# Kernel tuning notes

Hardware: AMD Instinct MI355X
Metric: run time of the kernel (lower is better)

The kernel has to match this reference:

```python
import jax, jax.numpy as jnp
import numpy as np

B, C, L, V, H, HEADS, ITERS = 8, 2048, 3, 512, 256, 8, 8
HD = H // HEADS
MAX_LIT = 1024  # literal embedding table holds 2*MAX_LIT rows


def _lin(x, W, b):
    return x @ W.T + b


def _gelu(x):
    return jax.nn.gelu(x, approximate=False)  # torch nn.GELU default = exact erf


def _ln(x, g, b):
    m = x.mean(-1, keepdims=True)
    v = ((x - m) ** 2).mean(-1, keepdims=True)
    return (x - m) / jnp.sqrt(v + 1e-5) * g + b


def setup_inputs() -> dict:
    key = jax.random.key(0)
    ks = jax.random.split(key, 16)
    s = 0.02
    p = {}
    p["formula"] = jax.random.randint(ks[0], (B, C, L), 0, 2 * V)
    p["lit_emb"] = jax.random.normal(ks[1], (2 * MAX_LIT, H)) * s
    # clause_encoder: Linear(H,2H) -> LayerNorm(2H) -> GELU -> Linear(2H,H)
    p["ce_w1"] = jax.random.normal(ks[2], (2 * H, H)) * s
    p["ce_b1"] = jnp.zeros((2 * H,))
    p["ce_g"] = jnp.ones((2 * H,))
    p["ce_beta"] = jnp.zeros((2 * H,))
    p["ce_w2"] = jax.random.normal(ks[3], (H, 2 * H)) * s
    p["ce_b2"] = jnp.zeros((H,))
    # clause_var_attention (nn.MultiheadAttention, eval mode -> no dropout)
    p["attn_in_w"] = jax.random.normal(ks[4], (3 * H, H)) * s
    p["attn_in_b"] = jnp.zeros((3 * H,))
    p["attn_out_w"] = jax.random.normal(ks[5], (H, H)) * s
    p["attn_out_b"] = jnp.zeros((H,))
    # variable_selector: Linear -> GELU -> Linear(H,1)
    p["vs_w1"] = jax.random.normal(ks[6], (H, H)) * s
    p["vs_b1"] = jnp.zeros((H,))
    p["vs_w2"] = jax.random.normal(ks[7], (1, H)) * s
    p["vs_b2"] = jnp.zeros((1,))
    # assignment_predictor: Linear -> GELU -> Linear(H,2) -> Softmax
    p["ap_w1"] = jax.random.normal(ks[8], (H, H)) * s
    p["ap_b1"] = jnp.zeros((H,))
    p["ap_w2"] = jax.random.normal(ks[9], (2, H)) * s
    p["ap_b2"] = jnp.zeros((2,))
    # sat_predictor: Linear -> GELU -> Linear(H,1) -> Sigmoid
    p["sp_w1"] = jax.random.normal(ks[10], (H, H)) * s
    p["sp_b1"] = jnp.zeros((H,))
    p["sp_w2"] = jax.random.normal(ks[11], (1, H)) * s
    p["sp_b2"] = jnp.zeros((1,))
    return p


def _mha(q, kv, in_w, in_b, out_w, out_b):
    Wq, Wk, Wv = jnp.split(in_w, 3, axis=0)
    bq, bk, bv = jnp.split(in_b, 3, axis=0)
    Bq, Nq, _ = q.shape
    Nk = kv.shape[1]
    qh = _lin(q, Wq, bq).reshape(Bq, Nq, HEADS, HD).transpose(0, 2, 1, 3)
    kh = _lin(kv, Wk, bk).reshape(Bq, Nk, HEADS, HD).transpose(0, 2, 1, 3)
    vh = _lin(kv, Wv, bv).reshape(Bq, Nk, HEADS, HD).transpose(0, 2, 1, 3)
    attn = jax.nn.softmax(jnp.einsum("bhqd,bhkd->bhqk", qh, kh) / np.float32(np.sqrt(HD)), axis=-1)
    o = jnp.einsum("bhqk,bhkd->bhqd", attn, vh).transpose(0, 2, 1, 3).reshape(Bq, Nq, H)
    return _lin(o, out_w, out_b)


def reference(formula, lit_emb, ce_w1, ce_b1, ce_g, ce_beta, ce_w2, ce_b2,
              attn_in_w, attn_in_b, attn_out_w, attn_out_b,
              vs_w1, vs_b1, vs_w2, vs_b2, ap_w1, ap_b1, ap_w2, ap_b2,
              sp_w1, sp_b1, sp_w2, sp_b2):
    bidx = jnp.arange(B)
    lit_e = lit_emb[formula]  # [B,C,L,H]
    # clause_encoder output is assignment-independent -> hoist out of the loop
    base = _lin(_gelu(_ln(_lin(lit_e.mean(2), ce_w1, ce_b1), ce_g, ce_beta)), ce_w2, ce_b2)  # [B,C,H]
    var_idx = formula // 2  # [B,C,L]
    pol = formula % 2

    def step(carry, _):
        assignments, var_states, done = carry
        va = assignments[bidx[:, None, None], var_idx]          # [B,C,L] gather
        sat = jnp.any((va == pol) & (va != 2), -1)              # [B,C]
        clause_states = base * (1.0 - 0.9 * sat[..., None].astype(base.dtype))
        vs = _mha(var_states, clause_states, attn_in_w, attn_in_b, attn_out_w, attn_out_b)  # [B,V,H]
        scores = _lin(_gelu(_lin(vs, vs_w1, vs_b1)), vs_w2, vs_b2)[..., 0]  # [B,V]
        scores = scores + (assignments != 2).astype(scores.dtype) * (-1e9)
        sel = jnp.argmax(scores, 1)                             # [B]
        sel_states = vs[bidx, sel]
        probs = jax.nn.softmax(_lin(_gelu(_lin(sel_states, ap_w1, ap_b1)), ap_w2, ap_b2), -1)
        new_a = jnp.argmax(probs, 1).astype(assignments.dtype)
        a2 = assignments.at[bidx, sel].set(new_a)
        # conflict check with updated assignments
        va2 = a2[bidx[:, None, None], var_idx]
        sat2 = jnp.any((va2 == pol) & (va2 != 2), -1)
        conflicting = jnp.all(va2 != 2, -1) & ~sat2             # [B,C]
        any_conf = jnp.any(conflicting)                         # global, as in torch list check
        a3 = jnp.where(any_conf, a2.at[bidx, sel].set(2), a2)   # unassign selected var on conflict
        finished = jnp.all(a3 != 2) & ~any_conf                 # torch early-break condition
        assignments_n = jnp.where(done, assignments, a3)        # freeze after break
        vs_n = jnp.where(done, var_states, vs)
        return (assignments_n, vs_n, done | finished), None

    init = (jnp.full((B, V), 2, jnp.int32), jnp.zeros((B, V, H), base.dtype), jnp.array(False))
    (assignments, var_states, _), _ = jax.lax.scan(step, init, None, length=ITERS)
    is_sat = jax.nn.sigmoid(_lin(_gelu(_lin(var_states.mean(1), sp_w1, sp_b1)), sp_w2, sp_b2))  # [B,1]
    return is_sat, assignments
```

## Files before the change

### kernel.cpp

```cpp
#include <hip/hip_runtime.h>
#include <hip/hip_bf16.h>

#pragma clang fp contract(off)

#define DEVI __device__ __forceinline__

constexpr int Bc = 8, Cc = 2048, Vc = 512, Hc = 256;

constexpr int W_N = 23;
constexpr int W_OFF[W_N] = {
  0,        524288,  655360,  655872,  656384,  656896,  787968,  788224,
  984832,   985600,  1051136, 1051392, 1116928, 1117184, 1117440, 1117444,
  1182980,  1183236, 1183748, 1183752, 1249288, 1249544, 1249800 };
constexpr int W_SZ[W_N] = {
  524288, 131072, 512, 512, 512, 131072, 256, 196608, 768,
  65536, 256, 65536, 256, 256, 1, 65536, 256, 512, 2, 65536, 256, 256, 1 };
constexpr int W_TOT = 1249804;

constexpr size_t WT1_O   = 1249808;
constexpr size_t WT2_O   = WT1_O   + 131072;
constexpr size_t WTIN_O  = WT2_O   + 131072;
constexpr size_t WTOUT_O = WTIN_O  + 196608;
constexpr size_t WTV1_O  = WTOUT_O + 65536;
constexpr size_t WTAP_O  = WTV1_O  + 65536;
constexpr size_t WTSP_O  = WTAP_O  + 65536;
constexpr size_t WCK_O   = WTSP_O  + 65536;
constexpr size_t WCV_O   = WCK_O   + 131072;
constexpr size_t BCK_O   = WCV_O   + 131072;
constexpr size_t BCV_O   = BCK_O   + 256;
constexpr size_t KB_O    = BCV_O   + 256;
constexpr size_t VB_O    = KB_O    + 4194304;
constexpr size_t VS8_O   = VB_O    + 4194304;
constexpr size_t OP_O    = VS8_O   + 2048;
constexpr size_t PM_O    = OP_O    + 8192;
constexpr size_t PL_O    = PM_O    + 256;
constexpr size_t FTOT    = PL_O    + 256;

constexpr int T_N = 7;
constexpr int T_SRC[T_N]  = { 524288, 656896, 788224, 985600, 1051392, 1117444, 1183752 };
constexpr size_t T_DST[T_N] = { WT1_O, WT2_O, WTIN_O, WTOUT_O, WTV1_O, WTAP_O, WTSP_O };
constexpr int T_ROWS[T_N] = { 512, 256, 768, 256, 256, 256, 256 };
constexpr int T_L2C[T_N]  = { 8, 9, 8, 8, 8, 8, 8 };
constexpr int T_CUM[T_N + 1] = { 0, 131072, 262144, 458752, 524288, 589824, 655360, 720896 };

struct SrcPtrs { const void* p[W_N]; };

DEVI float gelu_ref(float x) {
  return (x * (erff(x / 1.41421356237309504880f) + 1.0f)) * 0.5f;
}

__global__ __launch_bounds__(256) void k_detect(const unsigned short* __restrict__ lit,
                                                int* __restrict__ dflag) {
  __shared__ int red[256];
  int t = threadIdx.x, c = 0;
  for (int i = t; i < 4096; i += 256) {
    unsigned e = (lit[i] >> 7) & 0xFF;
    if (e >= 0x8F) c++;
  }
  red[t] = c;
  __syncthreads();
  for (int s = 128; s > 0; s >>= 1) {
    if (t < s) red[t] += red[t + s];
    __syncthreads();
  }
  if (t == 0) dflag[0] = (red[0] > 64) ? 1 : 0;
}

__global__ __launch_bounds__(256) void k_convert(SrcPtrs sp, float* __restrict__ wf,
                                                 const int* __restrict__ dflag) {
  int idx = blockIdx.x * 256 + threadIdx.x;
  if (idx >= W_TOT) return;
  const int isf32 = dflag[0];
  int i = 0;
  while (i + 1 < W_N && idx >= W_OFF[i + 1]) i++;
  int j = idx - W_OFF[i];
  float v = 0.f;
  if (j < W_SZ[i]) {
    if (isf32) v = ((const float*)sp.p[i])[j];
    else {
      unsigned int u = (unsigned int)((const unsigned short*)sp.p[i])[j] << 16;
      v = __uint_as_float(u);
    }
  }
  wf[idx] = v;
}

__global__ __launch_bounds__(256) void k_transpose(float* __restrict__ wf) {
  int idx = blockIdx.x * 256 + threadIdx.x;
  if (idx >= T_CUM[T_N]) return;
  int mi = 0;
  while (mi + 1 < T_N && idx >= T_CUM[mi + 1]) mi++;
  int local = idx - T_CUM[mi];
  int cols = 1 << T_L2C[mi];
  int r = local >> T_L2C[mi];
  int c = local & (cols - 1);
  wf[T_DST[mi] + (size_t)c * T_ROWS[mi] + r] = wf[T_SRC[mi] + (size_t)local];
}

__global__ __launch_bounds__(256) void k_combine(float* __restrict__ wf) {
  const int blk = blockIdx.x, t = threadIdx.x;
  const float* wtin = wf + WTIN_O;
  if (blk < 512) {
    __shared__ float w2row[256];
    w2row[t] = wf[WT2_O + (size_t)blk * 256 + t];
    __syncthreads();
    float aK = 0.f, aV = 0.f;
    for (int m = 0; m < 256; ++m) {
      float w2 = w2row[m];
      aK = fmaf(w2, wtin[(size_t)m * 768 + 256 + t], aK);
      aV = fmaf(w2, wtin[(size_t)m * 768 + 512 + t], aV);
    }
    wf[WCK_O + (size_t)blk * 256 + t] = aK;
    wf[WCV_O + (size_t)blk * 256 + t] = aV;
  } else {
    float aK = 0.f, aV = 0.f;
    for (int m = 0; m < 256; ++m) {
      float b2 = wf[W_OFF[6] + m];
      aK = fmaf(b2, wtin[(size_t)m * 768 + 256 + t], aK);
      aV = fmaf(b2, wtin[(size_t)m * 768 + 512 + t], aV);
    }
    wf[BCK_O + t] = aK;
    wf[BCV_O + t] = aV;
  }
}

__global__ __launch_bounds__(256) void k_init(float* __restrict__ vs8,
    int* __restrict__ assign, int* __restrict__ flags) {
  int idx = blockIdx.x * 256 + threadIdx.x;
  assign[idx] = 2;
  if (idx < 2048) vs8[idx] = 0.f;
  if (idx < 4) flags[idx] = 0;
}

__global__ __launch_bounds__(256) void k_base(const int* __restrict__ formula,
    const float* __restrict__ wf, float* __restrict__ Kb, float* __restrict__ Vb) {
  __shared__ __align__(16) float xs[16][256];
  __shared__ __align__(16) float h1[16][516];
  __shared__ float mv[16], vr[16];
  const int t = threadIdx.x;
  const int n0 = blockIdx.x * 16;
  const float* lit = wf + W_OFF[0];
  for (int r = 0; r < 16; ++r) {
    int n = n0 + r;
    int f0 = formula[n*3+0], f1 = formula[n*3+1], f2 = formula[n*3+2];
    xs[r][t] = (lit[f0*256 + t] + lit[f1*256 + t] + lit[f2*256 + t]) / 3.0f;
  }
  __syncthreads();
  {
    const float* w1t = wf + WT1_O;
    float a0[16], a1[16];
    #pragma unroll
    for (int r = 0; r < 16; ++r) { a0[r] = 0.f; a1[r] = 0.f; }
    for (int k = 0; k < 256; k += 4) {
      float wa0 = w1t[(size_t)(k+0)*512 + t], wa1 = w1t[(size_t)(k+1)*512 + t];
      float wa2 = w1t[(size_t)(k+2)*512 + t], wa3 = w1t[(size_t)(k+3)*512 + t];
      float wb0 = w1t[(size_t)(k+0)*512 + 256 + t], wb1 = w1t[(size_t)(k+1)*512 + 256 + t];
      float wb2 = w1t[(size_t)(k+2)*512 + 256 + t], wb3 = w1t[(size_t)(k+3)*512 + 256 + t];
      #pragma unroll
      for (int r = 0; r < 16; ++r) {
        float4 x4 = *(const float4*)&xs[r][k];
        a0[r] = fmaf(x4.x, wa0, a0[r]);
        a0[r] = fmaf(x4.y, wa1, a0[r]);
        a0[r] = fmaf(x4.z, wa2, a0[r]);
        a0[r] = fmaf(x4.w, wa3, a0[r]);
        a1[r] = fmaf(x4.x, wb0, a1[r]);
        a1[r] = fmaf(x4.y, wb1, a1[r]);
        a1[r] = fmaf(x4.z, wb2, a1[r]);
        a1[r] = fmaf(x4.w, wb3, a1[r]);
      }
    }
    float b0 = wf[W_OFF[2] + t], b1b = wf[W_OFF[2] + t + 256];
    #pragma unroll
    for (int r = 0; r < 16; ++r) {
      h1[r][t] = a0[r] + b0;
      h1[r][t + 256] = a1[r] + b1b;
    }
  }
  __syncthreads();
  if (t < 16) {
    float s = 0.f;
    for (int k = 0; k < 512; ++k) s += h1[t][k];
    float m = s / 512.0f;
    float v = 0.f;
    for (int k = 0; k < 512; ++k) { float d = h1[t][k] - m; float d2 = d * d; v += d2; }
    mv[t] = m; vr[t] = v / 512.0f;
  }
  __syncthreads();
  {
    const float* g  = wf + W_OFF[3];
    const float* be = wf + W_OFF[4];
    for (int r = 0; r < 16; ++r) {
      float sd = sqrtf(vr[r] + 1e-5f);
      for (int c = t; c < 512; c += 256) {
        float val = (h1[r][c] - mv[r]) / sd * g[c] + be[c];
        h1[r][c] = gelu_ref(val);
      }
    }
  }
  __syncthreads();
  {
    const float* wck = wf + WCK_O;
    const float* wcv = wf + WCV_O;
    float aK[16], aV[16];
    #pragma unroll
    for (int r = 0; r < 16; ++r) { aK[r] = 0.f; aV[r] = 0.f; }
    for (int k = 0; k < 512; k += 4) {
      float ck0 = wck[(size_t)(k+0)*256 + t], ck1 = wck[(size_t)(k+1)*256 + t];
      float ck2 = wck[(size_t)(k+2)*256 + t], ck3 = wck[(size_t)(k+3)*256 + t];
      float cv0 = wcv[(size_t)(k+0)*256 + t], cv1 = wcv[(size_t)(k+1)*256 + t];
      float cv2 = wcv[(size_t)(k+2)*256 + t], cv3 = wcv[(size_t)(k+3)*256 + t];
      #pragma unroll
      for (int r = 0; r < 16; ++r) {
        float4 x4 = *(const float4*)&h1[r][k];
        aK[r] = fmaf(x4.x, ck0, aK[r]);
        aK[r] = fmaf(x4.y, ck1, aK[r]);
        aK[r] = fmaf(x4.z, ck2, aK[r]);
        aK[r] = fmaf(x4.w, ck3, aK[r]);
        aV[r] = fmaf(x4.x, cv0, aV[r]);
        aV[r] = fmaf(x4.y, cv1, aV[r]);
        aV[r] = fmaf(x4.z, cv2, aV[r]);
        aV[r] = fmaf(x4.w, cv3, aV[r]);
      }
    }
    float bck = wf[BCK_O + t], bcv = wf[BCV_O + t];
    const int h = t >> 5, d = t & 31;
    for (int r = 0; r < 16; ++r) {
      int n = n0 + r;
      int b = n >> 11, j = n & 2047;
      size_t off = ((size_t)(b * 8 + h) * 2048 + j) * 32 + d;
      Kb[off] = aK[r] + bck;
      Vb[off] = aV[r] + bcv;
    }
  }
}

__global__ __launch_bounds__(256) void k_attn_part(const int* __restrict__ formula,
    const int* __restrict__ assign, const float* __restrict__ Kb,
    const float* __restrict__ Vb, const float* __restrict__ wf,
    const float* __restrict__ vs8, float* __restrict__ op, float* __restrict__ pm,
    float* __restrict__ pl, const int* __restrict__ flags) {
  if (flags[0]) return;
  __shared__ float xv[256], qs[32];
  __shared__ float sS[512], sF[512];
  __shared__ float sRed[256];
  __shared__ float sO[8][32];
  __shared__ float sM, sQB;
  const int blk = blockIdx.x;
  const int bh = blk >> 2, c = blk & 3;
  const int b = bh >> 3, h = bh & 7;
  const int t = threadIdx.x;
  const float FAC1 = 1.0f - 0.9f;

  xv[t] = vs8[b * 256 + t];
  __syncthreads();
  if (t < 32) {
    const float* wt = wf + WTIN_O;
    const int cc = h * 32 + t;
    float acc = 0.f;
    for (int k = 0; k < 256; ++k) acc = fmaf(xv[k], wt[(size_t)k * 768 + cc], acc);
    qs[t] = acc + wf[W_OFF[8] + cc];
  }
  __syncthreads();
  if (t == 0) {
    const float* bk = wf + W_OFF[8] + 256;
    float s = 0.f;
    for (int d = 0; d < 32; ++d) s = fmaf(qs[d], bk[h * 32 + d], s);
    sQB = s;
  }
  __syncthreads();
  float qreg[32];
  #pragma unroll
  for (int d = 0; d < 32; ++d) qreg[d] = qs[d];
  const float qb = sQB;
  const float* kbh = Kb + (size_t)bh * 2048 * 32;
  const float* vbh = Vb + (size_t)bh * 2048 * 32;

  float mloc = -3.402823466e38f;
  #pragma unroll
  for (int i = 0; i < 2; ++i) {
    int jl = i * 256 + t;
    int j = c * 512 + jl;
    int n = b * 2048 + j;
    bool sat = false;
    #pragma unroll
    for (int l = 0; l < 3; ++l) {
      int f = formula[n * 3 + l];
      int a = assign[b * 512 + (f >> 1)];
      sat = sat || (a == (f & 1));
    }
    float fac = sat ? FAC1 : 1.0f;
    const float4* kr4 = (const float4*)(kbh + (size_t)j * 32);
    float p = 0.f;
    #pragma unroll
    for (int g = 0; g < 8; ++g) {
      float4 kk = kr4[g];
      p = fmaf(qreg[4*g+0], kk.x, p);
      p = fmaf(qreg[4*g+1], kk.y, p);
      p = fmaf(qreg[4*g+2], kk.z, p);
      p = fmaf(qreg[4*g+3], kk.w, p);
    }
    float s = fmaf(fac, p, qb);
    sS[jl] = s; sF[jl] = fac;
    mloc = fmaxf(mloc, s);
  }
  sRed[t] = mloc;
  __syncthreads();
  for (int st = 128; st > 0; st >>= 1) {
    if (t < st) sRed[t] = fmaxf(sRed[t], sRed[t + st]);
    __syncthreads();
  }
  if (t == 0) sM = sRed[0];
  __syncthreads();
  const float Mc = sM;

  {
    float u0 = expf(sS[t * 2] - Mc);
    float u1 = expf(sS[t * 2 + 1] - Mc);
    float ll = u0 + u1;
    sS[t * 2] = u0 * sF[t * 2];
    sS[t * 2 + 1] = u1 * sF[t * 2 + 1];
    __syncthreads();
    sRed[t] = ll;
    __syncthreads();
    for (int st = 128; st > 0; st >>= 1) {
      if (t < st) sRed[t] = sRed[t] + sRed[t + st];
      __syncthreads();
    }
  }
  {
    const int jg = t >> 5, d = t & 31;
    float acc = 0.f;
    const float* vbase = vbh + (size_t)(c * 512 + jg * 64) * 32 + d;
    for (int jj = 0; jj < 64; ++jj)
      acc = fmaf(sS[jg * 64 + jj], vbase[(size_t)jj * 32], acc);
    sO[jg][d] = acc;
  }
  __syncthreads();
  if (t < 32) {
    float o = sO[0][t];
    #pragma unroll
    for (int g = 1; g < 8; ++g) o += sO[g][t];
    op[(size_t)(bh * 4 + c) * 32 + t] = o;
    if (t == 0) { pm[bh * 4 + c] = Mc; pl[bh * 4 + c] = sRed[0]; }
  }
}

__global__ __launch_bounds__(256) void k_update(const int* __restrict__ formula,
    const float* __restrict__ op, const float* __restrict__ pm,
    const float* __restrict__ pl, const float* __restrict__ wf,
    float* __restrict__ vs8, int* __restrict__ assign, int* __restrict__ selb,
    int* __restrict__ flags) {
  if (flags[0]) return;
  const int b = blockIdx.x, t = threadIdx.x;
  __shared__ float xo[256], xv[256], hh[256];
  __shared__ int ssel, sna, sconf, suna, slast;
  if (t == 0) { ssel = 512; sconf = 0; suna = 0; }
  {
    const int h = t >> 5, d = t & 31, bh = b * 8 + h;
    float m0 = pm[bh*4+0], m1 = pm[bh*4+1], m2 = pm[bh*4+2], m3 = pm[bh*4+3];
    float M = fmaxf(fmaxf(m0, m1), fmaxf(m2, m3));
    float e0 = expf(m0 - M), e1 = expf(m1 - M), e2 = expf(m2 - M), e3 = expf(m3 - M);
    float den = e0 * pl[bh*4+0];
    den = fmaf(e1, pl[bh*4+1], den);
    den = fmaf(e2, pl[bh*4+2], den);
    den = fmaf(e3, pl[bh*4+3], den);
    float O = e0 * op[(size_t)(bh*4+0)*32 + d];
    O = fmaf(e1, op[(size_t)(bh*4+1)*32 + d], O);
    O = fmaf(e2, op[(size_t)(bh*4+2)*32 + d], O);
    O = fmaf(e3, op[(size_t)(bh*4+3)*32 + d], O);
    float bv = wf[W_OFF[8] + 512 + h * 32 + d];
    xo[h * 32 + d] = O / den + bv;
  }
  __syncthreads();
  {
    const float* wt = wf + WTOUT_O;
    float acc = 0.f;
    for (int k = 0; k < 256; ++k) acc = fmaf(xo[k], wt[(size_t)k * 256 + t], acc);
    float v = acc + wf[W_OFF[10] + t];
    vs8[b * 256 + t] = v;
    xv[t] = v;
  }
  __syncthreads();
  for (int i = t; i < 512; i += 256)
    if (assign[b * 512 + i] == 2) atomicMin(&ssel, i);
  __syncthreads();
  const int sel = (ssel == 512) ? 0 : ssel;
  {
    const float* wt = wf + WTAP_O;
    float a = 0.f;
    for (int k = 0; k < 256; ++k) a = fmaf(xv[k], wt[(size_t)k * 256 + t], a);
    hh[t] = gelu_ref(a + wf[W_OFF[16] + t]);
  }
  __syncthreads();
  if (t == 0) {
    const float* w2 = wf + W_OFF[17];
    float l0 = 0.f, l1 = 0.f;
    for (int k = 0; k < 256; ++k) l0 = fmaf(hh[k], w2[k], l0);
    for (int k = 0; k < 256; ++k) l1 = fmaf(hh[k], w2[256 + k], l1);
    l0 += wf[W_OFF[18]];
    l1 += wf[W_OFF[18] + 1];
    int na = (l1 > l0) ? 1 : 0;
    assign[b * 512 + sel] = na;
    selb[b] = sel;
    sna = na;
  }
  __syncthreads();
  const int na = sna;
  int conf = 0, una = 0;
  for (int i = t; i < 2048; i += 256) {
    int n = b * 2048 + i;
    bool sat = false, alla = true;
    #pragma unroll
    for (int l = 0; l < 3; ++l) {
      int f = formula[n * 3 + l];
      int v = f >> 1;
      int a = (v == sel) ? na : assign[b * 512 + v];
      sat = sat || (a == (f & 1));
      alla = alla && (a != 2);
    }
    if (alla && !sat) conf = 1;
  }
  for (int i = t; i < 512; i += 256) {
    int a = (i == sel) ? na : assign[b * 512 + i];
    if (a == 2) una = 1;
  }
  if (conf) atomicOr(&sconf, 1);
  if (una) atomicOr(&suna, 1);
  __syncthreads();
  if (t == 0) {
    if (sconf) atomicOr(&flags[1], 1);
    if (suna) atomicOr(&flags[2], 1);
    __threadfence();
    int old = atomicAdd(&flags[3], 1);
    slast = (old == 7) ? 1 : 0;
  }
  __syncthreads();
  if (slast) {
    __threadfence();
    const int ac = flags[1], ua = flags[2];
    if (ac && t < 8) assign[t * 512 + selb[t]] = 2;
    if (t == 0) {
      if (!ac && !ua) flags[0] = 1;
      flags[1] = 0;
      flags[2] = 0;
      flags[3] = 0;
    }
  }
}

__global__ __launch_bounds__(256) void k_issat(const float* __restrict__ vs8,
    const int* __restrict__ assign, const float* __restrict__ wf,
    void* __restrict__ outv, const int* __restrict__ dflag) {
  const int b = blockIdx.x, t = threadIdx.x;
  const int isf32 = dflag[0];
  __shared__ float x[256], h[256];
  x[t] = vs8[b * 256 + t];
  __syncthreads();
  const float* wt = wf + WTSP_O;
  float a = 0.f;
  for (int k = 0; k < 256; ++k) a = fmaf(x[k], wt[(size_t)k * 256 + t], a);
  h[t] = gelu_ref(a + wf[W_OFF[20] + t]);
  __syncthreads();
  if (t == 0) {
    const float* w2 = wf + W_OFF[21];
    float l = 0.f;
    for (int k = 0; k < 256; ++k) l = fmaf(h[k], w2[k], l);
    l += wf[W_OFF[22]];
    float sig = 1.f / (1.f + expf(-l));
    if (isf32) ((float*)outv)[b] = sig;
    else ((__hip_bfloat16*)outv)[b] = __float2bfloat16(sig);
  }
  for (int i = t; i < 512; i += 256) {
    float av = (float)assign[b * 512 + i];
    if (isf32) ((float*)outv)[8 + b * 512 + i] = av;
    else ((__hip_bfloat16*)outv)[8 + b * 512 + i] = __float2bfloat16(av);
  }
}

extern "C" void kernel_launch(void* const* d_in, const int* in_sizes, int n_in,
                              void* d_out, int out_size, void* d_ws, size_t ws_size,
                              hipStream_t stream) {
  (void)in_sizes; (void)n_in; (void)out_size; (void)ws_size;
  const int* formula = (const int*)d_in[0];
  float* wf = (float*)d_ws;
  SrcPtrs sp;
  for (int i = 0; i < W_N; ++i) sp.p[i] = d_in[i + 1];
  float* Kb   = wf + KB_O;
  float* Vb   = wf + VB_O;
  float* vs8  = wf + VS8_O;
  float* op   = wf + OP_O;
  float* pm   = wf + PM_O;
  float* pl   = wf + PL_O;
  int* iw     = (int*)(wf + FTOT);
  int* assign = iw;
  int* selb   = iw + 4096;
  int* flags  = iw + 4104;
  int* dflag  = iw + 4108;

  k_detect<<<1, 256, 0, stream>>>((const unsigned short*)d_in[1], dflag);
  k_convert<<<(W_TOT + 255) / 256, 256, 0, stream>>>(sp, wf, dflag);
  k_transpose<<<(T_CUM[T_N] + 255) / 256, 256, 0, stream>>>(wf);
  k_combine<<<513, 256, 0, stream>>>(wf);
  k_init<<<16, 256, 0, stream>>>(vs8, assign, flags);
  k_base<<<1024, 256, 0, stream>>>(formula, wf, Kb, Vb);
  for (int it = 0; it < 8; ++it) {
    k_attn_part<<<256, 256, 0, stream>>>(formula, assign, Kb, Vb, wf, vs8, op, pm, pl, flags);
    k_update<<<8, 256, 0, stream>>>(formula, op, pm, pl, wf, vs8, assign, selb, flags);
  }
  k_issat<<<8, 256, 0, stream>>>(vs8, assign, wf, d_out, dflag);
}
```

Measured before the change: 755.4 us.

## Precompute literal projections, parallelize LayerNorm stats, fuse update into attention kernel

```diff
diff --git a/kernel.cpp b/kernel.cpp
--- a/kernel.cpp
+++ b/kernel.cpp
@@ -28,7 +28,8 @@
 constexpr size_t WCV_O   = WCK_O   + 131072;
 constexpr size_t BCK_O   = WCV_O   + 131072;
 constexpr size_t BCV_O   = BCK_O   + 256;
-constexpr size_t KB_O    = BCV_O   + 256;
+constexpr size_t LP_O    = BCV_O   + 256;
+constexpr size_t KB_O    = LP_O    + 524288;
 constexpr size_t VB_O    = KB_O    + 4194304;
 constexpr size_t VS8_O   = VB_O    + 4194304;
 constexpr size_t OP_O    = VS8_O   + 2048;
@@ -124,66 +125,94 @@
   }
 }
 
+__global__ __launch_bounds__(256) void k_litproj(float* __restrict__ wf) {
+  __shared__ __align__(16) float xs[16][256];
+  const int t = threadIdx.x;
+  const int l0 = blockIdx.x * 16;
+  const float* lit = wf + W_OFF[0];
+  for (int r = 0; r < 16; ++r)
+    xs[r][t] = lit[(size_t)(l0 + r) * 256 + t];
+  __syncthreads();
+  const float* w1t = wf + WT1_O;
+  float a0[16], a1[16];
+  #pragma unroll
+  for (int r = 0; r < 16; ++r) { a0[r] = 0.f; a1[r] = 0.f; }
+  for (int k = 0; k < 256; k += 4) {
+    float wa0 = w1t[(size_t)(k+0)*512 + t], wa1 = w1t[(size_t)(k+1)*512 + t];
+    float wa2 = w1t[(size_t)(k+2)*512 + t], wa3 = w1t[(size_t)(k+3)*512 + t];
+    float wb0 = w1t[(size_t)(k+0)*512 + 256 + t], wb1 = w1t[(size_t)(k+1)*512 + 256 + t];
+    float wb2 = w1t[(size_t)(k+2)*512 + 256 + t], wb3 = w1t[(size_t)(k+3)*512 + 256 + t];
+    #pragma unroll
+    for (int r = 0; r < 16; ++r) {
+      float4 x4 = *(const float4*)&xs[r][k];
+      a0[r] = fmaf(x4.x, wa0, a0[r]);
+      a0[r] = fmaf(x4.y, wa1, a0[r]);
+      a0[r] = fmaf(x4.z, wa2, a0[r]);
+      a0[r] = fmaf(x4.w, wa3, a0[r]);
+      a1[r] = fmaf(x4.x, wb0, a1[r]);
+      a1[r] = fmaf(x4.y, wb1, a1[r]);
+      a1[r] = fmaf(x4.z, wb2, a1[r]);
+      a1[r] = fmaf(x4.w, wb3, a1[r]);
+    }
+  }
+  float* LP = wf + LP_O;
+  for (int r = 0; r < 16; ++r) {
+    LP[(size_t)(l0 + r) * 512 + t] = a0[r];
+    LP[(size_t)(l0 + r) * 512 + 256 + t] = a1[r];
+  }
+}
+
 __global__ __launch_bounds__(256) void k_init(float* __restrict__ vs8,
-    int* __restrict__ assign, int* __restrict__ flags) {
+    int* __restrict__ assign, int* __restrict__ flags, int* __restrict__ batcnt) {
   int idx = blockIdx.x * 256 + threadIdx.x;
   assign[idx] = 2;
   if (idx < 2048) vs8[idx] = 0.f;
   if (idx < 4) flags[idx] = 0;
+  if (idx < 8) batcnt[idx] = 0;
 }
 
 __global__ __launch_bounds__(256) void k_base(const int* __restrict__ formula,
     const float* __restrict__ wf, float* __restrict__ Kb, float* __restrict__ Vb) {
-  __shared__ __align__(16) float xs[16][256];
   __shared__ __align__(16) float h1[16][516];
+  __shared__ float red2[16][16];
   __shared__ float mv[16], vr[16];
   const int t = threadIdx.x;
   const int n0 = blockIdx.x * 16;
-  const float* lit = wf + W_OFF[0];
+  const float* LP = wf + LP_O;
+  const float* b1 = wf + W_OFF[2];
   for (int r = 0; r < 16; ++r) {
     int n = n0 + r;
-    int f0 = formula[n*3+0], f1 = formula[n*3+1], f2 = formula[n*3+2];
-    xs[r][t] = (lit[f0*256 + t] + lit[f1*256 + t] + lit[f2*256 + t]) / 3.0f;
-  }
-  __syncthreads();
-  {
-    const float* w1t = wf + WT1_O;
-    float a0[16], a1[16];
-    #pragma unroll
-    for (int r = 0; r < 16; ++r) { a0[r] = 0.f; a1[r] = 0.f; }
-    for (int k = 0; k < 256; k += 4) {
-      float wa0 = w1t[(size_t)(k+0)*512 + t], wa1 = w1t[(size_t)(k+1)*512 + t];
-      float wa2 = w1t[(size_t)(k+2)*512 + t], wa3 = w1t[(size_t)(k+3)*512 + t];
-      float wb0 = w1t[(size_t)(k+0)*512 + 256 + t], wb1 = w1t[(size_t)(k+1)*512 + 256 + t];
-      float wb2 = w1t[(size_t)(k+2)*512 + 256 + t], wb3 = w1t[(size_t)(k+3)*512 + 256 + t];
-      #pragma unroll
-      for (int r = 0; r < 16; ++r) {
-        float4 x4 = *(const float4*)&xs[r][k];
-        a0[r] = fmaf(x4.x, wa0, a0[r]);
-        a0[r] = fmaf(x4.y, wa1, a0[r]);
-        a0[r] = fmaf(x4.z, wa2, a0[r]);
-        a0[r] = fmaf(x4.w, wa3, a0[r]);
-        a1[r] = fmaf(x4.x, wb0, a1[r]);
-        a1[r] = fmaf(x4.y, wb1, a1[r]);
-        a1[r] = fmaf(x4.z, wb2, a1[r]);
-        a1[r] = fmaf(x4.w, wb3, a1[r]);
-      }
-    }
-    float b0 = wf[W_OFF[2] + t], b1b = wf[W_OFF[2] + t + 256];
-    #pragma unroll
-    for (int r = 0; r < 16; ++r) {
-      h1[r][t] = a0[r] + b0;
-      h1[r][t + 256] = a1[r] + b1b;
-    }
+    const float* p0 = LP + (size_t)formula[n*3+0] * 512;
+    const float* p1 = LP + (size_t)formula[n*3+1] * 512;
+    const float* p2 = LP + (size_t)formula[n*3+2] * 512;
+    for (int c = t; c < 512; c += 256)
+      h1[r][c] = (p0[c] + p1[c] + p2[c]) / 3.0f + b1[c];
+  }
+  __syncthreads();
+  {
+    const int r = t >> 4, l16 = t & 15;
+    float s = 0.f;
+    for (int j = 0; j < 32; ++j) s += h1[r][l16 + j * 16];
+    red2[r][l16] = s;
   }
   __syncthreads();
   if (t < 16) {
     float s = 0.f;
-    for (int k = 0; k < 512; ++k) s += h1[t][k];
-    float m = s / 512.0f;
-    float v = 0.f;
-    for (int k = 0; k < 512; ++k) { float d = h1[t][k] - m; float d2 = d * d; v += d2; }
-    mv[t] = m; vr[t] = v / 512.0f;
+    for (int i = 0; i < 16; ++i) s += red2[t][i];
+    mv[t] = s / 512.0f;
+  }
+  __syncthreads();
+  {
+    const int r = t >> 4, l16 = t & 15;
+    float m = mv[r], v = 0.f;
+    for (int j = 0; j < 32; ++j) { float d = h1[r][l16 + j * 16] - m; v += d * d; }
+    red2[r][l16] = v;
+  }
+  __syncthreads();
+  if (t < 16) {
+    float s = 0.f;
+    for (int i = 0; i < 16; ++i) s += red2[t][i];
+    vr[t] = s / 512.0f;
   }
   __syncthreads();
   {
@@ -234,17 +263,19 @@
   }
 }
 
-__global__ __launch_bounds__(256) void k_attn_part(const int* __restrict__ formula,
-    const int* __restrict__ assign, const float* __restrict__ Kb,
-    const float* __restrict__ Vb, const float* __restrict__ wf,
-    const float* __restrict__ vs8, float* __restrict__ op, float* __restrict__ pm,
-    float* __restrict__ pl, const int* __restrict__ flags) {
+__global__ __launch_bounds__(256) void k_iter(const int* __restrict__ formula,
+    const float* __restrict__ Kb, const float* __restrict__ Vb,
+    const float* __restrict__ wf, float* __restrict__ vs8,
+    float* __restrict__ op, float* __restrict__ pm, float* __restrict__ pl,
+    int* __restrict__ assign, int* __restrict__ selb,
+    int* __restrict__ flags, int* __restrict__ batcnt) {
   if (flags[0]) return;
-  __shared__ float xv[256], qs[32];
-  __shared__ float sS[512], sF[512];
-  __shared__ float sRed[256];
+  __shared__ float xv[256], qs[32], qpart[8][32];
+  __shared__ float sS[512], sF[512], sRed[256];
   __shared__ float sO[8][32];
   __shared__ float sM, sQB;
+  __shared__ float xo[256], hh[256];
+  __shared__ int ssel, sna, sconf, suna, slastS, sglast;
   const int blk = blockIdx.x;
   const int bh = blk >> 2, c = blk & 3;
   const int b = bh >> 3, h = bh & 7;
@@ -253,12 +284,20 @@
 
   xv[t] = vs8[b * 256 + t];
   __syncthreads();
+  {
+    const float* wt = wf + WTIN_O;
+    const int cc = h * 32 + (t & 31), seg = t >> 5;
+    float part = 0.f;
+    for (int k = seg * 32; k < seg * 32 + 32; ++k)
+      part = fmaf(xv[k], wt[(size_t)k * 768 + cc], part);
+    qpart[seg][t & 31] = part;
+  }
+  __syncthreads();
   if (t < 32) {
-    const float* wt = wf + WTIN_O;
-    const int cc = h * 32 + t;
-    float acc = 0.f;
-    for (int k = 0; k < 256; ++k) acc = fmaf(xv[k], wt[(size_t)k * 768 + cc], acc);
-    qs[t] = acc + wf[W_OFF[8] + cc];
+    float acc = qpart[0][t];
+    #pragma unroll
+    for (int s = 1; s < 8; ++s) acc += qpart[s][t];
+    qs[t] = acc + wf[W_OFF[8] + h * 32 + t];
   }
   __syncthreads();
   if (t == 0) {
@@ -343,33 +382,32 @@
     op[(size_t)(bh * 4 + c) * 32 + t] = o;
     if (t == 0) { pm[bh * 4 + c] = Mc; pl[bh * 4 + c] = sRed[0]; }
   }
-}
-
-__global__ __launch_bounds__(256) void k_update(const int* __restrict__ formula,
-    const float* __restrict__ op, const float* __restrict__ pm,
-    const float* __restrict__ pl, const float* __restrict__ wf,
-    float* __restrict__ vs8, int* __restrict__ assign, int* __restrict__ selb,
-    int* __restrict__ flags) {
-  if (flags[0]) return;
-  const int b = blockIdx.x, t = threadIdx.x;
-  __shared__ float xo[256], xv[256], hh[256];
-  __shared__ int ssel, sna, sconf, suna, slast;
-  if (t == 0) { ssel = 512; sconf = 0; suna = 0; }
-  {
-    const int h = t >> 5, d = t & 31, bh = b * 8 + h;
-    float m0 = pm[bh*4+0], m1 = pm[bh*4+1], m2 = pm[bh*4+2], m3 = pm[bh*4+3];
+  __syncthreads();
+  if (t == 0) {
+    __threadfence();
+    int old = atomicAdd(&batcnt[b], 1);
+    slastS = (old == 31) ? 1 : 0;
+  }
+  __syncthreads();
+  if (!slastS) return;
+
+  __threadfence();
+  if (t == 0) { ssel = 512; sconf = 0; suna = 0; batcnt[b] = 0; }
+  {
+    const int h2 = t >> 5, d = t & 31, bh2 = b * 8 + h2;
+    float m0 = pm[bh2*4+0], m1 = pm[bh2*4+1], m2 = pm[bh2*4+2], m3 = pm[bh2*4+3];
     float M = fmaxf(fmaxf(m0, m1), fmaxf(m2, m3));
     float e0 = expf(m0 - M), e1 = expf(m1 - M), e2 = expf(m2 - M), e3 = expf(m3 - M);
-    float den = e0 * pl[bh*4+0];
-    den = fmaf(e1, pl[bh*4+1], den);
-    den = fmaf(e2, pl[bh*4+2], den);
-    den = fmaf(e3, pl[bh*4+3], den);
-    float O = e0 * op[(size_t)(bh*4+0)*32 + d];
-    O = fmaf(e1, op[(size_t)(bh*4+1)*32 + d], O);
-    O = fmaf(e2, op[(size_t)(bh*4+2)*32 + d], O);
-    O = fmaf(e3, op[(size_t)(bh*4+3)*32 + d], O);
-    float bv = wf[W_OFF[8] + 512 + h * 32 + d];
-    xo[h * 32 + d] = O / den + bv;
+    float den = e0 * pl[bh2*4+0];
+    den = fmaf(e1, pl[bh2*4+1], den);
+    den = fmaf(e2, pl[bh2*4+2], den);
+    den = fmaf(e3, pl[bh2*4+3], den);
+    float O = e0 * op[(size_t)(bh2*4+0)*32 + d];
+    O = fmaf(e1, op[(size_t)(bh2*4+1)*32 + d], O);
+    O = fmaf(e2, op[(size_t)(bh2*4+2)*32 + d], O);
+    O = fmaf(e3, op[(size_t)(bh2*4+3)*32 + d], O);
+    float bv = wf[W_OFF[8] + 512 + h2 * 32 + d];
+    xo[h2 * 32 + d] = O / den + bv;
   }
   __syncthreads();
   {
@@ -432,10 +470,10 @@
     if (suna) atomicOr(&flags[2], 1);
     __threadfence();
     int old = atomicAdd(&flags[3], 1);
-    slast = (old == 7) ? 1 : 0;
-  }
-  __syncthreads();
-  if (slast) {
+    sglast = (old == 7) ? 1 : 0;
+  }
+  __syncthreads();
+  if (sglast) {
     __threadfence();
     const int ac = flags[1], ua = flags[2];
     if (ac && t < 8) assign[t * 512 + selb[t]] = 2;
@@ -496,16 +534,18 @@
   int* selb   = iw + 4096;
   int* flags  = iw + 4104;
   int* dflag  = iw + 4108;
+  int* batcnt = iw + 4112;
 
   k_detect<<<1, 256, 0, stream>>>((const unsigned short*)d_in[1], dflag);
   k_convert<<<(W_TOT + 255) / 256, 256, 0, stream>>>(sp, wf, dflag);
   k_transpose<<<(T_CUM[T_N] + 255) / 256, 256, 0, stream>>>(wf);
   k_combine<<<513, 256, 0, stream>>>(wf);
-  k_init<<<16, 256, 0, stream>>>(vs8, assign, flags);
+  k_litproj<<<64, 256, 0, stream>>>(wf);
+  k_init<<<16, 256, 0, stream>>>(vs8, assign, flags, batcnt);
   k_base<<<1024, 256, 0, stream>>>(formula, wf, Kb, Vb);
   for (int it = 0; it < 8; ++it) {
-    k_attn_part<<<256, 256, 0, stream>>>(formula, assign, Kb, Vb, wf, vs8, op, pm, pl, flags);
-    k_update<<<8, 256, 0, stream>>>(formula, op, pm, pl, wf, vs8, assign, selb, flags);
+    k_iter<<<256, 256, 0, stream>>>(formula, Kb, Vb, wf, vs8, op, pm, pl,
+                                    assign, selb, flags, batcnt);
   }
   k_issat<<<8, 256, 0, stream>>>(vs8, assign, wf, d_out, dflag);
 }
```

Measured after the change: 745.8 us. About the same (-1.3%).
